# Kernel optimization log

Measured on AMD Instinct MI355X. Metric: run time of the kernel, lower is better.

## Reference

```python
import jax, jax.numpy as jnp
import numpy as np

B, N, E = 4, 8192, 65536
OBS, H, OUT, NOUT = 128, 256, 1024, 18


def setup_inputs() -> dict:
    key = jax.random.key(0)
    ks = jax.random.split(key, 8)
    nodes = jax.random.normal(ks[0], (B, N, OBS), dtype=jnp.float32)
    edges = jax.random.randint(ks[1], (B, 2, E), 0, N, dtype=jnp.int64)
    # Glorot-ish init for weights
    W0 = jax.random.normal(ks[2], (OBS, H), dtype=jnp.float32) / np.float32(np.sqrt(OBS))
    W1 = jax.random.normal(ks[3], (H, OUT), dtype=jnp.float32) / np.float32(np.sqrt(H))
    W_logit = jax.random.normal(ks[4], (OUT, NOUT), dtype=jnp.float32) / np.float32(np.sqrt(OUT))
    W_val = jax.random.normal(ks[5], (OUT, 1), dtype=jnp.float32) / np.float32(np.sqrt(OUT))
    return {
        "nodes": nodes, "edges": edges,
        "W0": W0, "b0": jnp.zeros((H,), jnp.float32),
        "W1": W1, "b1": jnp.zeros((OUT,), jnp.float32),
        "W_logit": W_logit, "b_logit": jnp.zeros((NOUT,), jnp.float32),
        "W_val": W_val, "b_val": jnp.zeros((1,), jnp.float32),
    }


def _gcn_layer(x, src, dst, W, b, n):
    # PyG GCNConv: out = D^{-1/2} (A + I) D^{-1/2} X W + b   (self-loops already in src/dst)
    h = x @ W                                                     # [N, F_out]
    deg = jax.ops.segment_sum(jnp.ones(src.shape, jnp.float32), dst, num_segments=n)
    dinv = jnp.where(deg > 0, jax.lax.rsqrt(deg), 0.0)            # deg^{-1/2}
    norm = dinv[src] * dinv[dst]                                  # [Etot]
    msg = h[src] * norm[:, None]                                  # gather + normalize
    agg = jax.ops.segment_sum(msg, dst, num_segments=n)           # scatter-add
    return agg + b


def reference(nodes, edges, W0, b0, W1, b1, W_logit, b_logit, W_val, b_val):
    n = nodes.shape[1]
    loops = jnp.arange(n, dtype=edges.dtype)  # self-loops, added by GCNConv

    def per_graph(x, ei):
        src = jnp.concatenate([ei[0], loops])
        dst = jnp.concatenate([ei[1], loops])
        h = jax.nn.relu(_gcn_layer(x, src, dst, W0, b0, n))
        # (original applies F.dropout here; omitted for a deterministic reference)
        h = jax.nn.relu(_gcn_layer(h, src, dst, W1, b1, n))
        return h

    out = jax.vmap(per_graph)(nodes, edges)        # [B, N, OUT]
    logits = out @ W_logit + b_logit               # [B, N, NOUT]
    values = (out @ W_val + b_val)[..., 0]         # [B, N]
    return logits, values
```

## Files before the change

kernel.cpp:

```cpp
#include <hip/hip_runtime.h>
#include <hip/hip_bf16.h>

#define BB   4
#define NN   8192
#define EE   65536
#define FOBS 128
#define FH   256
#define FOUT 1024
#define NLOG 18
#define P20  20
#define BKT  64

typedef __attribute__((ext_vector_type(8))) short frag8;
typedef __attribute__((ext_vector_type(4))) float f32x4;

__device__ __forceinline__ ushort f2b(float v) {
    __hip_bfloat16 h = __float2bfloat16(v);
    return *reinterpret_cast<ushort*>(&h);
}
__device__ __forceinline__ float blo(uint u) { return __uint_as_float(u << 16); }
__device__ __forceinline__ float bhi(uint u) { return __uint_as_float(u & 0xffff0000u); }

__device__ __forceinline__ void gld16(const void* g, void* l) {
    __builtin_amdgcn_global_load_lds(
        (const __attribute__((address_space(1))) unsigned*)g,
        (__attribute__((address_space(3))) unsigned*)l, 16, 0, 0);
}

#define W0_N   (FOBS * FH)
#define W1_N   (FH * FOUT)
#define WH_N   (19 * FOUT)
#define CUR_N  (BB * NN)
#define PREP_TOTAL (W0_N + W1_N + WH_N + CUR_N)

__global__ void prep_kernel(const float* __restrict__ W0, ushort* __restrict__ W0T,
                            const float* __restrict__ W1, ushort* __restrict__ W1T,
                            const float* __restrict__ Wl, const float* __restrict__ Wv,
                            ushort* __restrict__ WT19, int* __restrict__ cursor) {
    int idx = blockIdx.x * blockDim.x + threadIdx.x;
    if (idx < W0_N) {
        int n = idx / FOBS, k = idx - n * FOBS;
        W0T[idx] = f2b(W0[(size_t)k * FH + n]);
        return;
    }
    idx -= W0_N;
    if (idx < W1_N) {
        int n = idx / FH, k = idx - n * FH;
        W1T[idx] = f2b(W1[(size_t)k * FOUT + n]);
        return;
    }
    idx -= W1_N;
    if (idx < WH_N) {
        int o = idx >> 10, k = idx & (FOUT - 1);
        WT19[idx] = f2b((o < NLOG) ? Wl[(size_t)k * NLOG + o] : Wv[k]);
        return;
    }
    idx -= WH_N;
    if (idx < CUR_N) cursor[idx] = 0;
}

__global__ void bucket_fill(const int* __restrict__ edges, int* __restrict__ cursor,
                            int* __restrict__ bucket) {
    int blk = blockIdx.x;
    int xcd = blk & 7;
    int g = xcd >> 1;
    int chunk = (blk >> 3) * 2 + (xcd & 1);
    int e = chunk * 256 + threadIdx.x;
    const int* src = edges + (size_t)g * 2 * EE;
    const int* dst = src + EE;
    int d = dst[e];
    int slot = atomicAdd(&cursor[(size_t)g * NN + d], 1);
    if (slot < BKT) bucket[((size_t)g * NN + d) * BKT + slot] = src[e];
}

__global__ __launch_bounds__(256) void gather_agg_f32(
    const float* __restrict__ x_all, const int* __restrict__ cnt_all,
    const int* __restrict__ bucket, uint* __restrict__ agg_all)
{
    int g = blockIdx.y;
    int wv = threadIdx.x >> 6, lane = threadIdx.x & 63;
    int n = blockIdx.x * 4 + wv;
    const float2* x = (const float2*)(x_all + (size_t)g * NN * FOBS);
    const int* cnt = cnt_all + (size_t)g * NN;
    const int* bkt = bucket + ((size_t)g * NN + n) * BKT;

    int cn = cnt[n];
    float wn = rsqrtf((float)cn + 1.0f);
    int deg = min(cn, BKT);

    float2 self = x[(size_t)n * 64 + lane];
    float ax = wn * wn * self.x, ay = wn * wn * self.y;

    for (int i = 0; i < deg; i += 8) {
        int last = deg - 1;
        int s0 = bkt[i];
        int s1 = bkt[min(i + 1, last)], s2 = bkt[min(i + 2, last)], s3 = bkt[min(i + 3, last)];
        int s4 = bkt[min(i + 4, last)], s5 = bkt[min(i + 5, last)], s6 = bkt[min(i + 6, last)];
        int s7 = bkt[min(i + 7, last)];
        float w0 = rsqrtf((float)cnt[s0] + 1.0f) * wn;
        float w1 = (i + 1 < deg) ? rsqrtf((float)cnt[s1] + 1.0f) * wn : 0.0f;
        float w2 = (i + 2 < deg) ? rsqrtf((float)cnt[s2] + 1.0f) * wn : 0.0f;
        float w3 = (i + 3 < deg) ? rsqrtf((float)cnt[s3] + 1.0f) * wn : 0.0f;
        float w4 = (i + 4 < deg) ? rsqrtf((float)cnt[s4] + 1.0f) * wn : 0.0f;
        float w5 = (i + 5 < deg) ? rsqrtf((float)cnt[s5] + 1.0f) * wn : 0.0f;
        float w6 = (i + 6 < deg) ? rsqrtf((float)cnt[s6] + 1.0f) * wn : 0.0f;
        float w7 = (i + 7 < deg) ? rsqrtf((float)cnt[s7] + 1.0f) * wn : 0.0f;
        float2 r0 = x[(size_t)s0 * 64 + lane], r1 = x[(size_t)s1 * 64 + lane];
        float2 r2 = x[(size_t)s2 * 64 + lane], r3 = x[(size_t)s3 * 64 + lane];
        float2 r4 = x[(size_t)s4 * 64 + lane], r5 = x[(size_t)s5 * 64 + lane];
        float2 r6 = x[(size_t)s6 * 64 + lane], r7 = x[(size_t)s7 * 64 + lane];
        ax += w0 * r0.x + w1 * r1.x + w2 * r2.x + w3 * r3.x
            + w4 * r4.x + w5 * r5.x + w6 * r6.x + w7 * r7.x;
        ay += w0 * r0.y + w1 * r1.y + w2 * r2.y + w3 * r3.y
            + w4 * r4.y + w5 * r5.y + w6 * r6.y + w7 * r7.y;
    }
    agg_all[((size_t)g * NN + n) * 64 + lane] = (uint)f2b(ax) | ((uint)f2b(ay) << 16);
}

__global__ __launch_bounds__(256) void gather_agg_b256(
    const uint2* __restrict__ xb_all, const int* __restrict__ cnt_all,
    const int* __restrict__ bucket, uint2* __restrict__ agg_all)
{
    int g = blockIdx.y;
    int wv = threadIdx.x >> 6, lane = threadIdx.x & 63;
    int n = blockIdx.x * 4 + wv;
    const uint2* xb = xb_all + (size_t)g * NN * 64;
    const int* cnt = cnt_all + (size_t)g * NN;
    const int* bkt = bucket + ((size_t)g * NN + n) * BKT;

    int cn = cnt[n];
    float wn = rsqrtf((float)cn + 1.0f);
    int deg = min(cn, BKT);

    uint2 u = xb[(size_t)n * 64 + lane];
    float w2s = wn * wn;
    float a0 = w2s * blo(u.x), a1 = w2s * bhi(u.x), a2 = w2s * blo(u.y), a3 = w2s * bhi(u.y);

    for (int i = 0; i < deg; i += 8) {
        int last = deg - 1;
        int s0 = bkt[i];
        int s1 = bkt[min(i + 1, last)], s2 = bkt[min(i + 2, last)], s3 = bkt[min(i + 3, last)];
        int s4 = bkt[min(i + 4, last)], s5 = bkt[min(i + 5, last)], s6 = bkt[min(i + 6, last)];
        int s7 = bkt[min(i + 7, last)];
        float w0 = rsqrtf((float)cnt[s0] + 1.0f) * wn;
        float w1 = (i + 1 < deg) ? rsqrtf((float)cnt[s1] + 1.0f) * wn : 0.0f;
        float w2 = (i + 2 < deg) ? rsqrtf((float)cnt[s2] + 1.0f) * wn : 0.0f;
        float w3 = (i + 3 < deg) ? rsqrtf((float)cnt[s3] + 1.0f) * wn : 0.0f;
        float w4 = (i + 4 < deg) ? rsqrtf((float)cnt[s4] + 1.0f) * wn : 0.0f;
        float w5 = (i + 5 < deg) ? rsqrtf((float)cnt[s5] + 1.0f) * wn : 0.0f;
        float w6 = (i + 6 < deg) ? rsqrtf((float)cnt[s6] + 1.0f) * wn : 0.0f;
        float w7 = (i + 7 < deg) ? rsqrtf((float)cnt[s7] + 1.0f) * wn : 0.0f;
        uint2 r0 = xb[(size_t)s0 * 64 + lane], r1 = xb[(size_t)s1 * 64 + lane];
        uint2 r2 = xb[(size_t)s2 * 64 + lane], r3 = xb[(size_t)s3 * 64 + lane];
        uint2 r4 = xb[(size_t)s4 * 64 + lane], r5 = xb[(size_t)s5 * 64 + lane];
        uint2 r6 = xb[(size_t)s6 * 64 + lane], r7 = xb[(size_t)s7 * 64 + lane];
        a0 += w0 * blo(r0.x) + w1 * blo(r1.x) + w2 * blo(r2.x) + w3 * blo(r3.x)
            + w4 * blo(r4.x) + w5 * blo(r5.x) + w6 * blo(r6.x) + w7 * blo(r7.x);
        a1 += w0 * bhi(r0.x) + w1 * bhi(r1.x) + w2 * bhi(r2.x) + w3 * bhi(r3.x)
            + w4 * bhi(r4.x) + w5 * bhi(r5.x) + w6 * bhi(r6.x) + w7 * bhi(r7.x);
        a2 += w0 * blo(r0.y) + w1 * blo(r1.y) + w2 * blo(r2.y) + w3 * blo(r3.y)
            + w4 * blo(r4.y) + w5 * blo(r5.y) + w6 * blo(r6.y) + w7 * blo(r7.y);
        a3 += w0 * bhi(r0.y) + w1 * bhi(r1.y) + w2 * bhi(r2.y) + w3 * bhi(r3.y)
            + w4 * bhi(r4.y) + w5 * bhi(r5.y) + w6 * bhi(r6.y) + w7 * bhi(r7.y);
    }
    uint2 o;
    o.x = (uint)f2b(a0) | ((uint)f2b(a1) << 16);
    o.y = (uint)f2b(a2) | ((uint)f2b(a3) << 16);
    agg_all[((size_t)g * NN + n) * 64 + lane] = o;
}

__global__ __launch_bounds__(256) void mfma_gemm(
    const ushort* __restrict__ A_all, const ushort* __restrict__ BT,
    const float* __restrict__ bias, ushort* __restrict__ C_all,
    int M, int N, int K, int relu)
{
    __shared__ __align__(16) ushort As[128 * 64];
    __shared__ __align__(16) ushort Bs[128 * 64];

    int g = blockIdx.z;
    const ushort* A = A_all + (size_t)g * M * K;
    ushort* C = C_all + (size_t)g * M * N;

    int t = threadIdx.x;
    int bn = blockIdx.x, bm = blockIdx.y;
    int lane = t & 63, w = t >> 6;
    int wm = w >> 1, wn = w & 1;
    int l15 = lane & 15, quad = lane >> 4;

    f32x4 acc[4][4] = {};

    const char* Abase = (const char*)(A + (size_t)(bm * 128) * K);
    const char* Bbase = (const char*)(BT + (size_t)(bn * 128) * K);
    size_t rstride = (size_t)K * 2;

    int rsub = lane >> 3;
    int colb = (lane & 7) * 16;

    for (int k0 = 0; k0 < K; k0 += 64) {
#pragma unroll
        for (int c = 0; c < 4; ++c) {
            int grp = c * 4 + w;
            int row = grp * 8 + rsub;
            int gcol = k0 * 2 + (colb ^ ((row & 7) << 4));
            gld16(Abase + (size_t)row * rstride + gcol, (char*)As + grp * 1024);
            gld16(Bbase + (size_t)row * rstride + gcol, (char*)Bs + grp * 1024);
        }
        __syncthreads();
#pragma unroll
        for (int kk = 0; kk < 64; kk += 32) {
            frag8 af[4], bf[4];
#pragma unroll
            for (int i = 0; i < 4; ++i) {
                int r = wm * 64 + i * 16 + l15;
                int cb = (kk * 2 + quad * 16) ^ ((r & 7) << 4);
                af[i] = *(const frag8*)((const char*)As + r * 128 + cb);
            }
#pragma unroll
            for (int j = 0; j < 4; ++j) {
                int r = wn * 64 + j * 16 + l15;
                int cb = (kk * 2 + quad * 16) ^ ((r & 7) << 4);
                bf[j] = *(const frag8*)((const char*)Bs + r * 128 + cb);
            }
#pragma unroll
            for (int i = 0; i < 4; ++i)
#pragma unroll
                for (int j = 0; j < 4; ++j)
                    acc[i][j] = __builtin_amdgcn_mfma_f32_16x16x32_bf16(af[i], bf[j], acc[i][j], 0, 0, 0);
        }
        __syncthreads();
    }

#pragma unroll
    for (int i = 0; i < 4; ++i) {
#pragma unroll
        for (int j = 0; j < 4; ++j) {
            int col = bn * 128 + wn * 64 + j * 16 + l15;
            float bcol = bias[col];
#pragma unroll
            for (int r = 0; r < 4; ++r) {
                int row = bm * 128 + wm * 64 + i * 16 + quad * 4 + r;
                float v = acc[i][j][r] + bcol;
                if (relu) v = fmaxf(v, 0.0f);
                C[(size_t)row * N + col] = f2b(v);
            }
        }
    }
}

__global__ __launch_bounds__(256) void gemm2_heads(
    const ushort* __restrict__ hagg_all,
    const ushort* __restrict__ W1T,
    const float*  __restrict__ b1,
    const ushort* __restrict__ WT19,
    float* __restrict__ partial)
{
    __shared__ __align__(16) ushort smem[128 * 136];
    __shared__ __align__(16) ushort wt[20][136];

    char* AsB = (char*)smem;
    char* BsB = (char*)smem + 16384;
    ushort* Ct = smem;

    int bm = blockIdx.x, sp = blockIdx.y, g = blockIdx.z;
    int t = threadIdx.x;
    int lane = t & 63, w = t >> 6;
    int wm = w >> 1, wn = w & 1;
    int l15 = lane & 15, quad = lane >> 4;

    const char* A0 = (const char*)(hagg_all + ((size_t)g * NN + bm * 128) * FH);

    if (t < 136) wt[19][t] = 0;

    int rsub = lane >> 3;
    int colb = (lane & 7) * 16;

    f32x4 hacc[2][2] = {};

    for (int bi = 0; bi < 4; ++bi) {
        int bn = sp * 4 + bi;
        __syncthreads();

        for (int idx = t; idx < 19 * 16; idx += 256) {
            int row = idx >> 4, c8 = (idx & 15) * 8;
            *(uint4*)&wt[row][c8] = *(const uint4*)(WT19 + (size_t)row * FOUT + bn * 128 + c8);
        }

        f32x4 acc[4][4] = {};
        const char* Bbase = (const char*)(W1T + (size_t)(bn * 128) * FH);

        for (int k0 = 0; k0 < FH; k0 += 64) {
#pragma unroll
            for (int c = 0; c < 4; ++c) {
                int grp = c * 4 + w;
                int row = grp * 8 + rsub;
                int gcol = k0 * 2 + (colb ^ ((row & 7) << 4));
                gld16(A0 + (size_t)row * (FH * 2) + gcol, AsB + grp * 1024);
                gld16(Bbase + (size_t)row * (FH * 2) + gcol, BsB + grp * 1024);
            }
            __syncthreads();
#pragma unroll
            for (int kk = 0; kk < 64; kk += 32) {
                frag8 af[4], bf[4];
#pragma unroll
                for (int i = 0; i < 4; ++i) {
                    int r = wm * 64 + i * 16 + l15;
                    int cb = (kk * 2 + quad * 16) ^ ((r & 7) << 4);
                    af[i] = *(const frag8*)(AsB + r * 128 + cb);
                }
#pragma unroll
                for (int j = 0; j < 4; ++j) {
                    int r = wn * 64 + j * 16 + l15;
                    int cb = (kk * 2 + quad * 16) ^ ((r & 7) << 4);
                    bf[j] = *(const frag8*)(BsB + r * 128 + cb);
                }
#pragma unroll
                for (int i = 0; i < 4; ++i)
#pragma unroll
                    for (int j = 0; j < 4; ++j)
                        acc[i][j] = __builtin_amdgcn_mfma_f32_16x16x32_bf16(af[i], bf[j], acc[i][j], 0, 0, 0);
            }
            __syncthreads();
        }

#pragma unroll
        for (int j = 0; j < 4; ++j) {
            int colL = wn * 64 + j * 16 + l15;
            float bcol = b1[bn * 128 + colL];
#pragma unroll
            for (int i = 0; i < 4; ++i) {
                int rowL = wm * 64 + i * 16 + quad * 4;
#pragma unroll
                for (int r = 0; r < 4; ++r) {
                    float v = fmaxf(acc[i][j][r] + bcol, 0.0f);
                    Ct[(size_t)(rowL + r) * 136 + colL] = f2b(v);
                }
            }
        }
        __syncthreads();

        int r1 = (l15 < 3) ? (16 + l15) : 19;
#pragma unroll
        for (int kk = 0; kk < 128; kk += 32) {
            frag8 b0 = *(const frag8*)&wt[l15][kk + quad * 8];
            frag8 bO = *(const frag8*)&wt[r1][kk + quad * 8];
#pragma unroll
            for (int mt = 0; mt < 2; ++mt) {
                int row = (w * 2 + mt) * 16 + l15;
                frag8 af = *(const frag8*)&Ct[(size_t)row * 136 + kk + quad * 8];
                hacc[mt][0] = __builtin_amdgcn_mfma_f32_16x16x32_bf16(af, b0, hacc[mt][0], 0, 0, 0);
                hacc[mt][1] = __builtin_amdgcn_mfma_f32_16x16x32_bf16(af, bO, hacc[mt][1], 0, 0, 0);
            }
        }
    }

#pragma unroll
    for (int mt = 0; mt < 2; ++mt) {
#pragma unroll
        for (int r = 0; r < 4; ++r) {
            int node = bm * 128 + (w * 2 + mt) * 16 + quad * 4 + r;
            size_t base = ((size_t)(sp * BB + g) * NN + node) * P20;
            partial[base + l15] = hacc[mt][0][r];
            if (l15 < 3) partial[base + 16 + l15] = hacc[mt][1][r];
        }
    }
}

__global__ void heads_combine(const float* __restrict__ partial,
                              const float* __restrict__ bl, const float* __restrict__ bv,
                              float* __restrict__ out_logits, float* __restrict__ out_values) {
    int i = blockIdx.x * blockDim.x + threadIdx.x;
    if (i >= BB * NN * 19) return;
    int o = i % 19;
    int gn = i / 19;
    float v = partial[(size_t)gn * P20 + o] + partial[((size_t)BB * NN + gn) * P20 + o];
    if (o < NLOG) out_logits[(size_t)gn * NLOG + o] = v + bl[o];
    else          out_values[gn] = v + bv[0];
}

extern "C" void kernel_launch(void* const* d_in, const int* in_sizes, int n_in,
                              void* d_out, int out_size, void* d_ws, size_t ws_size,
                              hipStream_t stream) {
    const float* nodes = (const float*)d_in[0];
    const int*   edges = (const int*)d_in[1];
    const float* W0 = (const float*)d_in[2];
    const float* b0 = (const float*)d_in[3];
    const float* W1 = (const float*)d_in[4];
    const float* b1 = (const float*)d_in[5];
    const float* Wl = (const float*)d_in[6];
    const float* bl = (const float*)d_in[7];
    const float* Wv = (const float*)d_in[8];
    const float* bv = (const float*)d_in[9];

    float* out_logits = (float*)d_out;
    float* out_values = out_logits + (size_t)BB * NN * NLOG;

    char* ws = (char*)d_ws;
    int*    cursor  = (int*)(ws);
    ushort* W0T     = (ushort*)(ws + (128 << 10));
    ushort* W1T     = (ushort*)(ws + (192 << 10));
    ushort* WT19    = (ushort*)(ws + (704 << 10));
    int*    bucket  = (int*)(ws + (1u << 20));
    ushort* xagg_b  = (ushort*)(ws + (9u << 20));
    ushort* h1b     = (ushort*)(ws + (17u << 20));
    ushort* hagg_b  = (ushort*)(ws + (33u << 20));
    float*  partial = (float*)(ws + (49u << 20));

    prep_kernel<<<(PREP_TOTAL + 255) / 256, 256, 0, stream>>>(
        W0, W0T, W1, W1T, Wl, Wv, WT19, cursor);

    bucket_fill<<<1024, 256, 0, stream>>>(edges, cursor, bucket);

    gather_agg_f32<<<dim3(NN / 4, BB), 256, 0, stream>>>(nodes, cursor, bucket, (uint*)xagg_b);

    mfma_gemm<<<dim3(FH / 128, NN / 128, BB), 256, 0, stream>>>(
        xagg_b, W0T, b0, h1b, NN, FH, FOBS, 1);

    gather_agg_b256<<<dim3(NN / 4, BB), 256, 0, stream>>>((const uint2*)h1b, cursor, bucket,
                                                          (uint2*)hagg_b);

    gemm2_heads<<<dim3(NN / 128, 2, BB), 256, 0, stream>>>(hagg_b, W1T, b1, WT19, partial);

    heads_combine<<<(BB * NN * 19 + 255) / 256, 256, 0, stream>>>(partial, bl, bv,
                                                                  out_logits, out_values);
}
```

Before: 187.6 us.

## Fold head reduction into atomics and remap gather blocks per XCD

Removes the heads_combine kernel. Bias initialisation of the outputs moves into prep_kernel, and gemm2_heads atomically adds its two split-K partial results straight into the logits and values. Both gather kernels switch to a 1D grid whose block index maps each graph to a pair of XCDs, so each graph's feature rows stay in fewer L2 caches. This saves one launch and the partial-buffer round trip, at the cost of float atomics, which make the summation order nondeterministic.

```diff
diff --git a/kernel.cpp b/kernel.cpp
--- a/kernel.cpp
+++ b/kernel.cpp
@@ -8,7 +8,6 @@
 #define FH   256
 #define FOUT 1024
 #define NLOG 18
-#define P20  20
 #define BKT  64
 
 typedef __attribute__((ext_vector_type(8))) short frag8;
@@ -31,12 +30,15 @@
 #define W1_N   (FH * FOUT)
 #define WH_N   (19 * FOUT)
 #define CUR_N  (BB * NN)
-#define PREP_TOTAL (W0_N + W1_N + WH_N + CUR_N)
+#define OUTI_N (BB * NN * 19)
+#define PREP_TOTAL (W0_N + W1_N + WH_N + CUR_N + OUTI_N)
 
 __global__ void prep_kernel(const float* __restrict__ W0, ushort* __restrict__ W0T,
                             const float* __restrict__ W1, ushort* __restrict__ W1T,
                             const float* __restrict__ Wl, const float* __restrict__ Wv,
-                            ushort* __restrict__ WT19, int* __restrict__ cursor) {
+                            ushort* __restrict__ WT19, int* __restrict__ cursor,
+                            const float* __restrict__ bl, const float* __restrict__ bv,
+                            float* __restrict__ out_logits, float* __restrict__ out_values) {
     int idx = blockIdx.x * blockDim.x + threadIdx.x;
     if (idx < W0_N) {
         int n = idx / FOBS, k = idx - n * FOBS;
@@ -56,7 +58,13 @@
         return;
     }
     idx -= WH_N;
-    if (idx < CUR_N) cursor[idx] = 0;
+    if (idx < CUR_N) { cursor[idx] = 0; return; }
+    idx -= CUR_N;
+    if (idx < OUTI_N) {
+        int gn = idx / 19, o = idx - gn * 19;
+        if (o < NLOG) out_logits[(size_t)gn * NLOG + o] = bl[o];
+        else          out_values[gn] = bv[0];
+    }
 }
 
 __global__ void bucket_fill(const int* __restrict__ edges, int* __restrict__ cursor,
@@ -77,9 +85,12 @@
     const float* __restrict__ x_all, const int* __restrict__ cnt_all,
     const int* __restrict__ bucket, uint* __restrict__ agg_all)
 {
-    int g = blockIdx.y;
+    int blk = blockIdx.x;
+    int xcd = blk & 7;
+    int g = xcd >> 1;
+    int chunk = (blk >> 3) * 2 + (xcd & 1);
     int wv = threadIdx.x >> 6, lane = threadIdx.x & 63;
-    int n = blockIdx.x * 4 + wv;
+    int n = chunk * 4 + wv;
     const float2* x = (const float2*)(x_all + (size_t)g * NN * FOBS);
     const int* cnt = cnt_all + (size_t)g * NN;
     const int* bkt = bucket + ((size_t)g * NN + n) * BKT;
@@ -121,9 +132,12 @@
     const uint2* __restrict__ xb_all, const int* __restrict__ cnt_all,
     const int* __restrict__ bucket, uint2* __restrict__ agg_all)
 {
-    int g = blockIdx.y;
+    int blk = blockIdx.x;
+    int xcd = blk & 7;
+    int g = xcd >> 1;
+    int chunk = (blk >> 3) * 2 + (xcd & 1);
     int wv = threadIdx.x >> 6, lane = threadIdx.x & 63;
-    int n = blockIdx.x * 4 + wv;
+    int n = chunk * 4 + wv;
     const uint2* xb = xb_all + (size_t)g * NN * 64;
     const int* cnt = cnt_all + (size_t)g * NN;
     const int* bkt = bucket + ((size_t)g * NN + n) * BKT;
@@ -252,7 +266,8 @@
     const ushort* __restrict__ W1T,
     const float*  __restrict__ b1,
     const ushort* __restrict__ WT19,
-    float* __restrict__ partial)
+    float* __restrict__ out_logits,
+    float* __restrict__ out_values)
 {
     __shared__ __align__(16) ushort smem[128 * 136];
     __shared__ __align__(16) ushort wt[20][136];
@@ -358,23 +373,12 @@
 #pragma unroll
         for (int r = 0; r < 4; ++r) {
             int node = bm * 128 + (w * 2 + mt) * 16 + quad * 4 + r;
-            size_t base = ((size_t)(sp * BB + g) * NN + node) * P20;
-            partial[base + l15] = hacc[mt][0][r];
-            if (l15 < 3) partial[base + 16 + l15] = hacc[mt][1][r];
-        }
-    }
-}
-
-__global__ void heads_combine(const float* __restrict__ partial,
-                              const float* __restrict__ bl, const float* __restrict__ bv,
-                              float* __restrict__ out_logits, float* __restrict__ out_values) {
-    int i = blockIdx.x * blockDim.x + threadIdx.x;
-    if (i >= BB * NN * 19) return;
-    int o = i % 19;
-    int gn = i / 19;
-    float v = partial[(size_t)gn * P20 + o] + partial[((size_t)BB * NN + gn) * P20 + o];
-    if (o < NLOG) out_logits[(size_t)gn * NLOG + o] = v + bl[o];
-    else          out_values[gn] = v + bv[0];
+            size_t gn = (size_t)g * NN + node;
+            atomicAdd(&out_logits[gn * NLOG + l15], hacc[mt][0][r]);
+            if (l15 < 2)       atomicAdd(&out_logits[gn * NLOG + 16 + l15], hacc[mt][1][r]);
+            else if (l15 == 2) atomicAdd(&out_values[gn], hacc[mt][1][r]);
+        }
+    }
 }
 
 extern "C" void kernel_launch(void* const* d_in, const int* in_sizes, int n_in,
@@ -403,23 +407,20 @@
     ushort* xagg_b  = (ushort*)(ws + (9u << 20));
     ushort* h1b     = (ushort*)(ws + (17u << 20));
     ushort* hagg_b  = (ushort*)(ws + (33u << 20));
-    float*  partial = (float*)(ws + (49u << 20));
 
     prep_kernel<<<(PREP_TOTAL + 255) / 256, 256, 0, stream>>>(
-        W0, W0T, W1, W1T, Wl, Wv, WT19, cursor);
+        W0, W0T, W1, W1T, Wl, Wv, WT19, cursor, bl, bv, out_logits, out_values);
 
     bucket_fill<<<1024, 256, 0, stream>>>(edges, cursor, bucket);
 
-    gather_agg_f32<<<dim3(NN / 4, BB), 256, 0, stream>>>(nodes, cursor, bucket, (uint*)xagg_b);
+    gather_agg_f32<<<(NN / 4) * BB, 256, 0, stream>>>(nodes, cursor, bucket, (uint*)xagg_b);
 
     mfma_gemm<<<dim3(FH / 128, NN / 128, BB), 256, 0, stream>>>(
         xagg_b, W0T, b0, h1b, NN, FH, FOBS, 1);
 
-    gather_agg_b256<<<dim3(NN / 4, BB), 256, 0, stream>>>((const uint2*)h1b, cursor, bucket,
-                                                          (uint2*)hagg_b);
-
-    gemm2_heads<<<dim3(NN / 128, 2, BB), 256, 0, stream>>>(hagg_b, W1T, b1, WT19, partial);
-
-    heads_combine<<<(BB * NN * 19 + 255) / 256, 256, 0, stream>>>(partial, bl, bv,
-                                                                  out_logits, out_values);
-}
+    gather_agg_b256<<<(NN / 4) * BB, 256, 0, stream>>>((const uint2*)h1b, cursor, bucket,
+                                                       (uint2*)hagg_b);
+
+    gemm2_heads<<<dim3(NN / 128, 2, BB), 256, 0, stream>>>(hagg_b, W1T, b1, WT19,
+                                                           out_logits, out_values);
+}
```

Measured after the change: 187.5 us. Within noise of the previous version (-0.0%).
